# Kernel optimization log

Hardware: AMD Instinct MI355X
Metric: run time of the kernel (lower is better)

Reference implementation:

```python
import jax, jax.numpy as jnp
import numpy as np

STATE = 256
IN = 128
OUT = 128


def setup_inputs() -> dict:
    key = jax.random.key(0)
    ks = jax.random.split(key, 10)
    u = jax.random.normal(ks[0], (8, 2048, IN), dtype=jnp.float32)
    x0_re = jax.random.normal(ks[1], (8, STATE), dtype=jnp.float32)
    x0_im = jax.random.normal(ks[2], (8, STATE), dtype=jnp.float32)
    # A init: 2*pi*rand angles on unit circle, scaled by 10 (enforce_stability=True)
    theta = 2.0 * jnp.pi * jax.random.uniform(ks[3], (STATE,), dtype=jnp.float32)
    A_re = 10.0 * jnp.cos(theta)
    A_im = 10.0 * jnp.sin(theta)
    # complex randn: real/imag parts each have variance 1/2
    inv_sqrt2 = 1.0 / np.sqrt(2.0)
    sB = inv_sqrt2 / np.sqrt(STATE + IN)
    B_re = jax.random.normal(ks[4], (IN, STATE), dtype=jnp.float32) * sB
    B_im = jax.random.normal(ks[5], (IN, STATE), dtype=jnp.float32) * sB
    sC = inv_sqrt2 / np.sqrt(STATE + OUT)
    C_re = jax.random.normal(ks[6], (STATE, OUT), dtype=jnp.float32) * sC
    C_im = jax.random.normal(ks[7], (STATE, OUT), dtype=jnp.float32) * sC
    D = jnp.zeros((IN, OUT), dtype=jnp.float32)
    b = jnp.zeros((OUT,), dtype=jnp.float32)
    return {"u": u, "x0_re": x0_re, "x0_im": x0_im, "A_re": A_re, "A_im": A_im,
            "B_re": B_re, "B_im": B_im, "C_re": C_re, "C_im": C_im, "D": D, "b": b}


def reference(u, x0_re, x0_im, A_re, A_im, B_re, B_im, C_re, C_im, D, b):
    cdt = jnp.complex64
    length = u.shape[1]
    A = (A_re + 1j * A_im).astype(cdt)
    # enforce_stability: map poles inside unit disc
    A = A / jnp.sqrt(A * jnp.conj(A) + 1.0)
    # Vandermonde powers A^t for t in [0, length]  -> [length+1, n]
    Aps = A[None, :] ** jnp.arange(length + 1)[:, None]
    Bm = (B_re + 1j * B_im).astype(cdt)
    uB = u.astype(cdt) @ Bm  # [batch, length, n]
    # FFT-based causal convolution of Aps[:-1] ([length, n]) with uB
    T = 2 ** int(np.ceil(np.log2(2 * length - 1)))
    AF = jnp.fft.fft(Aps[:-1], n=T, axis=0)      # [T, n]
    UF = jnp.fft.fft(uB, n=T, axis=1)            # [batch, T, n]
    x = jnp.fft.ifft(AF[None] * UF, axis=1)[:, :length]  # [batch, length, n]
    # add initial-state contribution A^t * x0
    x0 = (x0_re + 1j * x0_im).astype(cdt)
    x = x + Aps[1:][None] * x0[:, None, :]
    Cm = (C_re + 1j * C_im).astype(cdt)
    y = jnp.real(x @ Cm) + u @ D + b
    return y, x[:, -1]
```

## Files before the change

kernel.cpp:

```cpp
#include <hip/hip_runtime.h>
#include <math.h>

#define BATCH 8
#define T 2048
#define N 256
#define INF 128
#define OUTF 128
#define L 16
#define LOG2L 4
#define NC (T / L)
#define KTOT 640
#define NKS 20
#define NKU 4
#define UBS 516

typedef __attribute__((ext_vector_type(8))) short short8;
typedef __attribute__((ext_vector_type(4))) float f32x4;

__device__ __forceinline__ unsigned short f2b(float f) {
    union { float f; unsigned u; } x; x.f = f;
    unsigned r = (x.u + 0x7FFFu + ((x.u >> 16) & 1u)) >> 16;
    return (unsigned short)r;
}
__device__ __forceinline__ float b2f(unsigned short s) {
    union { unsigned u; float f; } x; x.u = ((unsigned)s) << 16;
    return x.f;
}

__global__ __launch_bounds__(256) void k_prep(const float* __restrict__ Are,
                                              const float* __restrict__ Aim,
                                              const float* __restrict__ Bre,
                                              const float* __restrict__ Bim,
                                              const float* __restrict__ Cre,
                                              const float* __restrict__ Cim,
                                              const float* __restrict__ D,
                                              float2* __restrict__ Apow,
                                              unsigned short* __restrict__ Bswz,
                                              unsigned short* __restrict__ Bswz2) {
    int blk = blockIdx.x;
    int tid = threadIdx.x;
    if (blk < 40) {
        int unit = blk * 4 + (tid >> 6);
        int ks = unit >> 3, ot = unit & 7;
        int l = tid & 63;
        int o = ot * 16 + (l & 15);
        int k0 = ks * 32 + (l >> 4) * 8;
        short8 out;
#pragma unroll
        for (int j = 0; j < 8; ++j) {
            int gk = k0 + j;
            float v = (gk < 256) ? Cre[gk * OUTF + o]
                    : (gk < 512) ? -Cim[(gk - 256) * OUTF + o]
                                 : D[(gk - 512) * OUTF + o];
            out[j] = (short)f2b(v);
        }
        *(short8*)(Bswz + ((size_t)unit * 64 + l) * 8) = out;
    } else if (blk < 72) {
        int unit = (blk - 40) * 4 + (tid >> 6);
        int l = tid & 63;
        int col = (unit & 31) * 16 + (l & 15);
        int k0 = (unit >> 5) * 32 + (l >> 4) * 8;
        short8 out;
#pragma unroll
        for (int j = 0; j < 8; ++j) {
            int gk = k0 + j;
            float v = (col < 256) ? Bre[gk * N + col] : Bim[gk * N + col - 256];
            out[j] = (short)f2b(v);
        }
        *(short8*)(Bswz2 + ((size_t)unit * 64 + l) * 8) = out;
    } else {
        int n = tid;
        float ar = Are[n], ai = Aim[n];
        float inv = 1.0f / sqrtf(ar * ar + ai * ai + 1.0f);
        ar *= inv; ai *= inv;
        float pr = ar, pi = ai;
        for (int j = 0; j < L; ++j) {
            Apow[j * N + n] = make_float2(pr, pi);
            float nr = pr * ar - pi * ai;
            float ni = pr * ai + pi * ar;
            pr = nr; pi = ni;
        }
    }
}

__global__ __launch_bounds__(512, 8) void kU_scan(const float* __restrict__ u,
                                                  const unsigned short* __restrict__ Bswz2,
                                                  const float2* __restrict__ Apow,
                                                  unsigned short* __restrict__ xbb,
                                                  float2* __restrict__ carr) {
    __shared__ float uB[16][UBS];
    int tid = threadIdx.x;
    int lane = tid & 63;
    int w = tid >> 6;
    size_t rowg0 = (size_t)blockIdx.x * 16;
    const float* uprow = u + (rowg0 + (lane & 15)) * INF + (lane >> 4) * 8;

    f32x4 acc[4];
#pragma unroll
    for (int i = 0; i < 4; ++i) acc[i] = (f32x4){0.f, 0.f, 0.f, 0.f};

    const short8* Bfr2 = (const short8*)Bswz2;
#pragma unroll
    for (int ks = 0; ks < NKU; ++ks) {
        float4 a0 = *(const float4*)(uprow + ks * 32);
        float4 a1 = *(const float4*)(uprow + ks * 32 + 4);
        short8 af;
        af[0] = (short)f2b(a0.x); af[1] = (short)f2b(a0.y);
        af[2] = (short)f2b(a0.z); af[3] = (short)f2b(a0.w);
        af[4] = (short)f2b(a1.x); af[5] = (short)f2b(a1.y);
        af[6] = (short)f2b(a1.z); af[7] = (short)f2b(a1.w);
#pragma unroll
        for (int i = 0; i < 4; ++i) {
            int ct = w * 4 + i;
            short8 bf = Bfr2[(size_t)(ks * 32 + ct) * 64 + lane];
            acc[i] = __builtin_amdgcn_mfma_f32_16x16x32_bf16(af, bf, acc[i], 0, 0, 0);
        }
    }
    {
        int rbase = (lane >> 4) * 4;
        int cb = lane & 15;
#pragma unroll
        for (int i = 0; i < 4; ++i) {
            int col = (w * 4 + i) * 16 + cb;
#pragma unroll
            for (int r = 0; r < 4; ++r)
                uB[rbase + r][col] = acc[i][r];
        }
    }
    __syncthreads();

    if (tid < 256) {
        int n = tid;
        int b = (int)(rowg0 >> 11);
        int c = (int)((rowg0 & 2047) >> LOG2L);
        float2 a = Apow[n];
        float xr = 0.f, xi = 0.f;
#pragma unroll
        for (int j = 0; j < 16; ++j) {
            float ur = uB[j][n];
            float ui = uB[j][256 + n];
            float nr = fmaf(a.x, xr, fmaf(-a.y, xi, ur));
            float ni = fmaf(a.x, xi, fmaf(a.y, xr, ui));
            xr = nr; xi = ni;
            size_t rowg = rowg0 + j;
            xbb[rowg * 512 + n]       = f2b(xr);
            xbb[rowg * 512 + 256 + n] = f2b(xi);
        }
        carr[((size_t)b * NC + c) * N + n] = make_float2(xr, xi);
    }
}

__global__ __launch_bounds__(256) void k2_carry(const float* __restrict__ x0re,
                                                const float* __restrict__ x0im,
                                                const float2* __restrict__ Apow,
                                                float2* __restrict__ carr,
                                                float* __restrict__ out_tail,
                                                int tail_mode) {
    int b = blockIdx.x, n = threadIdx.x;
    float pr = x0re[b * N + n], pi = x0im[b * N + n];
    float2 aL = Apow[(L - 1) * N + n];
#pragma unroll 8
    for (int c = 0; c < NC; ++c) {
        size_t off = ((size_t)b * NC + c) * N + n;
        float2 f = carr[off];
        carr[off] = make_float2(pr, pi);
        float nr = f.x + aL.x * pr - aL.y * pi;
        float ni = f.y + aL.x * pi + aL.y * pr;
        pr = nr; pi = ni;
    }
    if (tail_mode == 2) {
        out_tail[(b * N + n) * 2 + 0] = pr;
        out_tail[(b * N + n) * 2 + 1] = pi;
    } else if (tail_mode == 1) {
        out_tail[b * N + n] = pr;
    }
}

__global__ __launch_bounds__(256) void k3_mfma(const unsigned short* __restrict__ xbb,
                                               const float2* __restrict__ Apow,
                                               const float2* __restrict__ carr,
                                               const float* __restrict__ u,
                                               const unsigned short* __restrict__ Bswz,
                                               const float* __restrict__ bias,
                                               float* __restrict__ y) {
    int tid = threadIdx.x;
    int lane = tid & 63;
    int w = tid >> 6;
    size_t rowg = (size_t)blockIdx.x * 64 + w * 16 + (lane & 15);
    int koff = (lane >> 4) * 8;
    int t = (int)(rowg & 2047);
    int b = (int)(rowg >> 11);
    int j = t & (L - 1);
    int c = t >> LOG2L;
    const float4* Ap4 = (const float4*)(Apow + (size_t)j * N);
    const float4* Cv4 = (const float4*)(carr + ((size_t)b * NC + c) * N);
    const unsigned short* arow = xbb + rowg * 512 + koff;
    const float* urow = u + rowg * INF + koff;
    const short8* Bfr = (const short8*)Bswz;

    f32x4 acc[8];
#pragma unroll
    for (int ot = 0; ot < 8; ++ot) acc[ot] = (f32x4){0.f, 0.f, 0.f, 0.f};

#pragma unroll 2
    for (int g = 0; g < 8; ++g) {
        short8 xre = *(const short8*)(arow + g * 32);
        short8 xim = *(const short8*)(arow + (g + 8) * 32);
        int n0 = g * 32 + koff;
        float4 ap[4], vv[4];
#pragma unroll
        for (int q = 0; q < 4; ++q) {
            ap[q] = Ap4[(n0 >> 1) + q];
            vv[q] = Cv4[(n0 >> 1) + q];
        }
        short8 afr, afi;
#pragma unroll
        for (int e = 0; e < 8; ++e) {
            float4 aq = ap[e >> 1];
            float4 vq = vv[e >> 1];
            float pr = (e & 1) ? aq.z : aq.x;
            float pi = (e & 1) ? aq.w : aq.y;
            float vr = (e & 1) ? vq.z : vq.x;
            float vi = (e & 1) ? vq.w : vq.y;
            afr[e] = (short)f2b(b2f((unsigned short)xre[e]) + (pr * vr - pi * vi));
            afi[e] = (short)f2b(b2f((unsigned short)xim[e]) + (pr * vi + pi * vr));
        }
#pragma unroll
        for (int ot = 0; ot < 8; ++ot) {
            short8 bf = Bfr[((size_t)g * 8 + ot) * 64 + lane];
            acc[ot] = __builtin_amdgcn_mfma_f32_16x16x32_bf16(afr, bf, acc[ot], 0, 0, 0);
        }
#pragma unroll
        for (int ot = 0; ot < 8; ++ot) {
            short8 bf = Bfr[((size_t)(g + 8) * 8 + ot) * 64 + lane];
            acc[ot] = __builtin_amdgcn_mfma_f32_16x16x32_bf16(afi, bf, acc[ot], 0, 0, 0);
        }
    }
#pragma unroll
    for (int ks2 = 0; ks2 < 4; ++ks2) {
        float4 a0 = *(const float4*)(urow + ks2 * 32);
        float4 a1 = *(const float4*)(urow + ks2 * 32 + 4);
        short8 af;
        af[0] = (short)f2b(a0.x); af[1] = (short)f2b(a0.y);
        af[2] = (short)f2b(a0.z); af[3] = (short)f2b(a0.w);
        af[4] = (short)f2b(a1.x); af[5] = (short)f2b(a1.y);
        af[6] = (short)f2b(a1.z); af[7] = (short)f2b(a1.w);
#pragma unroll
        for (int ot = 0; ot < 8; ++ot) {
            short8 bf = Bfr[((size_t)(16 + ks2) * 8 + ot) * 64 + lane];
            acc[ot] = __builtin_amdgcn_mfma_f32_16x16x32_bf16(af, bf, acc[ot], 0, 0, 0);
        }
    }

    int colb = lane & 15;
    int rq = lane >> 4;
    size_t rowout = (size_t)blockIdx.x * 64 + w * 16 + rq * 4;
#pragma unroll
    for (int ot = 0; ot < 8; ++ot) {
        int o = ot * 16 + colb;
        float bv = bias[o];
#pragma unroll
        for (int r = 0; r < 4; ++r) {
            y[(rowout + r) * OUTF + o] = acc[ot][r] + bv;
        }
    }
}

extern "C" void kernel_launch(void* const* d_in, const int* in_sizes, int n_in,
                              void* d_out, int out_size, void* d_ws, size_t ws_size,
                              hipStream_t stream) {
    const float* u    = (const float*)d_in[0];
    const float* x0re = (const float*)d_in[1];
    const float* x0im = (const float*)d_in[2];
    const float* Are  = (const float*)d_in[3];
    const float* Aim  = (const float*)d_in[4];
    const float* Bre  = (const float*)d_in[5];
    const float* Bim  = (const float*)d_in[6];
    const float* Cre  = (const float*)d_in[7];
    const float* Cim  = (const float*)d_in[8];
    const float* D    = (const float*)d_in[9];
    const float* bias = (const float*)d_in[10];
    float* y = (float*)d_out;

    char* ws = (char*)d_ws;
    float2* Apow = (float2*)ws;
    char* p = ws + (size_t)L * N * sizeof(float2);
    float2* carr = (float2*)p;
    p += (size_t)BATCH * NC * N * sizeof(float2);
    unsigned short* xbb = (unsigned short*)p;
    p += (size_t)BATCH * T * 512 * sizeof(unsigned short);
    unsigned short* Bswz = (unsigned short*)p;
    p += (size_t)NKS * 8 * 64 * 8 * sizeof(unsigned short);
    unsigned short* Bswz2 = (unsigned short*)p;

    const int ysz = BATCH * T * OUTF;
    const int tail_elems = out_size - ysz;
    int tail_mode = (tail_elems >= BATCH * N * 2) ? 2
                  : (tail_elems >= BATCH * N) ? 1 : 0;
    float* tail = y + ysz;

    k_prep<<<73, 256, 0, stream>>>(Are, Aim, Bre, Bim, Cre, Cim, D, Apow, Bswz, Bswz2);
    kU_scan<<<BATCH * NC, 512, 0, stream>>>(u, Bswz2, Apow, xbb, carr);
    k2_carry<<<BATCH, 256, 0, stream>>>(x0re, x0im, Apow, carr, tail, tail_mode);
    k3_mfma<<<(BATCH * T) / 64, 256, 0, stream>>>(xbb, Apow, carr, u, Bswz, bias, y);
}
```

Measured before the change: 62.13 us.

## Stage B fragments in double-buffered LDS across the k3 MFMA loop

```diff
diff --git a/kernel.cpp b/kernel.cpp
--- a/kernel.cpp
+++ b/kernel.cpp
@@ -183,6 +183,7 @@
                                                const unsigned short* __restrict__ Bswz,
                                                const float* __restrict__ bias,
                                                float* __restrict__ y) {
+    __shared__ short8 Bs[2][1024];
     int tid = threadIdx.x;
     int lane = tid & 63;
     int w = tid >> 6;
@@ -202,54 +203,89 @@
 #pragma unroll
     for (int ot = 0; ot < 8; ++ot) acc[ot] = (f32x4){0.f, 0.f, 0.f, 0.f};
 
-#pragma unroll 2
-    for (int g = 0; g < 8; ++g) {
-        short8 xre = *(const short8*)(arow + g * 32);
-        short8 xim = *(const short8*)(arow + (g + 8) * 32);
-        int n0 = g * 32 + koff;
-        float4 ap[4], vv[4];
+    auto KApair = [](int p, int& ka, int& kb) {
+        if (p < 8) { ka = p; kb = p + 8; }
+        else if (p == 8) { ka = 16; kb = 17; }
+        else { ka = 18; kb = 19; }
+    };
+
+    short8 st[4];
+    auto LOADB = [&](int p) {
+        int ka, kb; KApair(p, ka, kb);
 #pragma unroll
         for (int q = 0; q < 4; ++q) {
-            ap[q] = Ap4[(n0 >> 1) + q];
-            vv[q] = Cv4[(n0 >> 1) + q];
-        }
-        short8 afr, afi;
-#pragma unroll
-        for (int e = 0; e < 8; ++e) {
-            float4 aq = ap[e >> 1];
-            float4 vq = vv[e >> 1];
-            float pr = (e & 1) ? aq.z : aq.x;
-            float pi = (e & 1) ? aq.w : aq.y;
-            float vr = (e & 1) ? vq.z : vq.x;
-            float vi = (e & 1) ? vq.w : vq.y;
-            afr[e] = (short)f2b(b2f((unsigned short)xre[e]) + (pr * vr - pi * vi));
-            afi[e] = (short)f2b(b2f((unsigned short)xim[e]) + (pr * vi + pi * vr));
-        }
+            int slot = tid * 4 + q;
+            int kk = slot >> 9;
+            int rem = slot & 511;
+            st[q] = Bfr[(size_t)(kk ? kb : ka) * 512 + rem];
+        }
+    };
+    auto WRITEB = [&](int buf) {
+#pragma unroll
+        for (int q = 0; q < 4; ++q) Bs[buf][tid * 4 + q] = st[q];
+    };
+
+    LOADB(0);
+    WRITEB(0);
+    __syncthreads();
+
+    int cur = 0;
+    for (int p = 0; p < 10; ++p) {
+        if (p < 9) LOADB(p + 1);
+
+        short8 afa, afb;
+        if (p < 8) {
+            short8 xre = *(const short8*)(arow + p * 32);
+            short8 xim = *(const short8*)(arow + (p + 8) * 32);
+            int n0 = p * 32 + koff;
+            float4 ap[4], vv[4];
+#pragma unroll
+            for (int q = 0; q < 4; ++q) {
+                ap[q] = Ap4[(n0 >> 1) + q];
+                vv[q] = Cv4[(n0 >> 1) + q];
+            }
+#pragma unroll
+            for (int e = 0; e < 8; ++e) {
+                float4 aq = ap[e >> 1];
+                float4 vq = vv[e >> 1];
+                float pr = (e & 1) ? aq.z : aq.x;
+                float pi = (e & 1) ? aq.w : aq.y;
+                float vr = (e & 1) ? vq.z : vq.x;
+                float vi = (e & 1) ? vq.w : vq.y;
+                afa[e] = (short)f2b(b2f((unsigned short)xre[e]) + (pr * vr - pi * vi));
+                afb[e] = (short)f2b(b2f((unsigned short)xim[e]) + (pr * vi + pi * vr));
+            }
+        } else {
+            int ks2a = (p == 8) ? 0 : 2;
+            float4 a0 = *(const float4*)(urow + ks2a * 32);
+            float4 a1 = *(const float4*)(urow + ks2a * 32 + 4);
+            afa[0] = (short)f2b(a0.x); afa[1] = (short)f2b(a0.y);
+            afa[2] = (short)f2b(a0.z); afa[3] = (short)f2b(a0.w);
+            afa[4] = (short)f2b(a1.x); afa[5] = (short)f2b(a1.y);
+            afa[6] = (short)f2b(a1.z); afa[7] = (short)f2b(a1.w);
+            float4 b0 = *(const float4*)(urow + (ks2a + 1) * 32);
+            float4 b1 = *(const float4*)(urow + (ks2a + 1) * 32 + 4);
+            afb[0] = (short)f2b(b0.x); afb[1] = (short)f2b(b0.y);
+            afb[2] = (short)f2b(b0.z); afb[3] = (short)f2b(b0.w);
+            afb[4] = (short)f2b(b1.x); afb[5] = (short)f2b(b1.y);
+            afb[6] = (short)f2b(b1.z); afb[7] = (short)f2b(b1.w);
+        }
+
 #pragma unroll
         for (int ot = 0; ot < 8; ++ot) {
-            short8 bf = Bfr[((size_t)g * 8 + ot) * 64 + lane];
-            acc[ot] = __builtin_amdgcn_mfma_f32_16x16x32_bf16(afr, bf, acc[ot], 0, 0, 0);
+            short8 bf = Bs[cur][ot * 64 + lane];
+            acc[ot] = __builtin_amdgcn_mfma_f32_16x16x32_bf16(afa, bf, acc[ot], 0, 0, 0);
         }
 #pragma unroll
         for (int ot = 0; ot < 8; ++ot) {
-            short8 bf = Bfr[((size_t)(g + 8) * 8 + ot) * 64 + lane];
-            acc[ot] = __builtin_amdgcn_mfma_f32_16x16x32_bf16(afi, bf, acc[ot], 0, 0, 0);
-        }
-    }
-#pragma unroll
-    for (int ks2 = 0; ks2 < 4; ++ks2) {
-        float4 a0 = *(const float4*)(urow + ks2 * 32);
-        float4 a1 = *(const float4*)(urow + ks2 * 32 + 4);
-        short8 af;
-        af[0] = (short)f2b(a0.x); af[1] = (short)f2b(a0.y);
-        af[2] = (short)f2b(a0.z); af[3] = (short)f2b(a0.w);
-        af[4] = (short)f2b(a1.x); af[5] = (short)f2b(a1.y);
-        af[6] = (short)f2b(a1.z); af[7] = (short)f2b(a1.w);
-#pragma unroll
-        for (int ot = 0; ot < 8; ++ot) {
-            short8 bf = Bfr[((size_t)(16 + ks2) * 8 + ot) * 64 + lane];
-            acc[ot] = __builtin_amdgcn_mfma_f32_16x16x32_bf16(af, bf, acc[ot], 0, 0, 0);
-        }
+            short8 bf = Bs[cur][512 + ot * 64 + lane];
+            acc[ot] = __builtin_amdgcn_mfma_f32_16x16x32_bf16(afb, bf, acc[ot], 0, 0, 0);
+        }
+
+        __syncthreads();
+        if (p < 9) WRITEB(cur ^ 1);
+        __syncthreads();
+        cur ^= 1;
     }
 
     int colb = lane & 15;
```

Measured after the change: 55.49 us. -10.7%, faster.
